# Optimization experiments

Hardware: AMD Instinct MI355X
Metric: run time of the kernel (lower is better)

The kernel has to match this reference:

```python
import jax, jax.numpy as jnp
import numpy as np

# Inverse Haar synthesis filters [LL, LH, HL, HH], each 2x2, shape [4,2,2]
_INV_FILTERS = jnp.array([
    [[0.5, 0.5], [0.5, 0.5]],    # LL
    [[-0.5, -0.5], [0.5, 0.5]],  # LH
    [[-0.5, 0.5], [-0.5, 0.5]],  # HL
    [[0.5, -0.5], [-0.5, 0.5]],  # HH
], dtype=jnp.float32)


def _iwt(ll, hf, filt):
    # ll: [B,C,H,W]; hf: [B,3C,H,W] -> recon [B,C,2H,2W]
    B, C, H, W = ll.shape
    # interleave: per channel c -> [ll_c, hf_{3c..3c+2}*2-1], shape [B,C,4,H,W]
    res = jnp.concatenate([ll[:, :, None], hf.reshape(B, C, 3, H, W) * 2.0 - 1.0], axis=2)
    # stride-2 2x2 transpose conv == scatter each pixel into a 2x2 block
    out = jnp.einsum('bckhw,kpq->bchpwq', res, filt)  # [B,C,H,2,W,2]
    return out.reshape(B, C, 2 * H, 2 * W)


def setup_inputs() -> dict:
    key = jax.random.key(0)
    k1, k2, k3, k4 = jax.random.split(key, 4)
    B, in_ch = 16, 64
    fused = jax.random.normal(k1, (B, in_ch, 128, 128), dtype=jnp.float32)
    hf1 = jax.random.uniform(k2, (B, 9, 256, 256), dtype=jnp.float32)
    hf2 = jax.random.uniform(k3, (B, 9, 128, 128), dtype=jnp.float32)
    conv_w = jax.random.normal(k4, (3, in_ch, 3, 3), dtype=jnp.float32) * 0.05
    conv_b = jnp.zeros((3,), dtype=jnp.float32)
    return {"fused": fused, "hf1": hf1, "hf2": hf2, "conv_w": conv_w, "conv_b": conv_b}


def reference(fused, hf1, hf2, conv_w, conv_b):
    # recov: Conv2d(in_ch, 3, 3, padding=1) + Tanh
    y = jax.lax.conv_general_dilated(
        fused, conv_w, window_strides=(1, 1), padding=((1, 1), (1, 1)),
        dimension_numbers=('NCHW', 'OIHW', 'NCHW'))
    ll_ref = jnp.tanh(y + conv_b[None, :, None, None])  # [B,3,128,128]
    # multi_iwt over reversed coeffs: curr starts at coarsest ll (= ll_ref)
    curr = _iwt(ll_ref, hf2, _INV_FILTERS)  # [B,3,256,256]
    curr = _iwt(curr, hf1, _INV_FILTERS)    # [B,3,512,512]
    return curr
```

## Files before the change

kernel.cpp:

```cpp
#include <hip/hip_runtime.h>
#include <cmath>


#define H1 128
#define W1 128
#define H2 256
#define W2 256
#define H3 512
#define W3 512
#define IN_CH 64

__global__ __launch_bounds__(256) void conv_tanh_kernel(
    const float* __restrict__ fused,
    const float* __restrict__ cw,
    const float* __restrict__ cb,
    float* __restrict__ ll)
{
    const int tx = threadIdx.x;
    const int ty = threadIdx.y;
    const int h  = blockIdx.y * 4 + ty;
    const int b  = blockIdx.z;
    const int w0 = tx * 2;

    float acc[3][2];
    #pragma unroll
    for (int oc = 0; oc < 3; ++oc) { acc[oc][0] = 0.f; acc[oc][1] = 0.f; }

    const float* fb = fused + ((size_t)b * IN_CH) * H1 * W1;

    for (int ic = 0; ic < IN_CH; ++ic) {
        const float* fc = fb + ic * H1 * W1;
        float v[3][4];
        #pragma unroll
        for (int r = 0; r < 3; ++r) {
            const int hh = h + r - 1;
            const bool hv = (hh >= 0) && (hh < H1);
            const float* row = fc + hh * W1;
            v[r][0] = (hv && (w0 > 0)) ? row[w0 - 1] : 0.f;
            if (hv) {
                float2 m = *(const float2*)(row + w0);
                v[r][1] = m.x; v[r][2] = m.y;
            } else {
                v[r][1] = 0.f; v[r][2] = 0.f;
            }
            v[r][3] = (hv && ((w0 + 2) < W1)) ? row[w0 + 2] : 0.f;
        }
        #pragma unroll
        for (int oc = 0; oc < 3; ++oc) {
            const float* wp = cw + (oc * IN_CH + ic) * 9;
            #pragma unroll
            for (int kh = 0; kh < 3; ++kh) {
                #pragma unroll
                for (int kw = 0; kw < 3; ++kw) {
                    const float wv = wp[kh * 3 + kw];
                    acc[oc][0] = fmaf(v[kh][kw],     wv, acc[oc][0]);
                    acc[oc][1] = fmaf(v[kh][kw + 1], wv, acc[oc][1]);
                }
            }
        }
    }

    #pragma unroll
    for (int oc = 0; oc < 3; ++oc) {
        const float bv = cb[oc];
        float2 o;
        o.x = tanhf(acc[oc][0] + bv);
        o.y = tanhf(acc[oc][1] + bv);
        *(float2*)(ll + (((size_t)b * 3 + oc) * H1 + h) * W1 + w0) = o;
    }
}

__global__ __launch_bounds__(256) void iwt2_kernel(
    const float* __restrict__ ll,
    const float* __restrict__ hf2,
    const float* __restrict__ hf1,
    float* __restrict__ out)
{
    const int idx = blockIdx.x * 256 + threadIdx.x;
    const int w = idx & (W1 - 1);
    const int h = (idx >> 7) & (H1 - 1);
    const int rest = idx >> 14;
    const int c = rest % 3;
    const int b = rest / 3;

    const float llv = ll[(((size_t)b * 3 + c) * H1 + h) * W1 + w];

    const float* h2p = hf2 + (((size_t)b * 9 + 3 * c) * H1 + h) * W1 + w;
    const float a2 = h2p[0]           * 2.f - 1.f;
    const float b2 = h2p[H1 * W1]     * 2.f - 1.f;
    const float c2 = h2p[2 * H1 * W1] * 2.f - 1.f;

    float mid[2][2];
    mid[0][0] = 0.5f * (llv - a2 - b2 + c2);
    mid[0][1] = 0.5f * (llv - a2 + b2 - c2);
    mid[1][0] = 0.5f * (llv + a2 - b2 - c2);
    mid[1][1] = 0.5f * (llv + a2 + b2 + c2);

    const float* h1b = hf1 + ((size_t)b * 9 + 3 * c) * H2 * W2;
    float* ob = out + (((size_t)b * 3 + c) * H3) * W3;

    #pragma unroll
    for (int p = 0; p < 2; ++p) {
        const int Hr = 2 * h + p;
        const float* rowp = h1b + Hr * W2 + 2 * w;
        const float2 a1 = *(const float2*)(rowp);
        const float2 b1 = *(const float2*)(rowp + H2 * W2);
        const float2 c1 = *(const float2*)(rowp + 2 * H2 * W2);
        const float ax = a1.x * 2.f - 1.f, ay = a1.y * 2.f - 1.f;
        const float bx = b1.x * 2.f - 1.f, by = b1.y * 2.f - 1.f;
        const float cx = c1.x * 2.f - 1.f, cy = c1.y * 2.f - 1.f;
        #pragma unroll
        for (int r = 0; r < 2; ++r) {
            const float sr = r ? 1.f : -1.f;
            float4 o;
            o.x = 0.5f * (mid[p][0] + sr * ax - bx - sr * cx);
            o.y = 0.5f * (mid[p][0] + sr * ax + bx + sr * cx);
            o.z = 0.5f * (mid[p][1] + sr * ay - by - sr * cy);
            o.w = 0.5f * (mid[p][1] + sr * ay + by + sr * cy);
            *(float4*)(ob + (4 * h + 2 * p + r) * W3 + 4 * w) = o;
        }
    }
}

extern "C" void kernel_launch(void* const* d_in, const int* in_sizes, int n_in,
                              void* d_out, int out_size, void* d_ws, size_t ws_size,
                              hipStream_t stream) {
    (void)in_sizes; (void)n_in; (void)out_size; (void)ws_size;
    const float* fused = (const float*)d_in[0];
    const float* hf1   = (const float*)d_in[1];
    const float* hf2   = (const float*)d_in[2];
    const float* cw    = (const float*)d_in[3];
    const float* cb    = (const float*)d_in[4];
    float* out = (float*)d_out;
    float* ll  = (float*)d_ws;

    dim3 cblk(64, 4, 1);
    dim3 cgrd(1, H1 / 4, 16);
    conv_tanh_kernel<<<cgrd, cblk, 0, stream>>>(fused, cw, cb, ll);

    const int total = 16 * 3 * H1 * W1;
    iwt2_kernel<<<total / 256, 256, 0, stream>>>(ll, hf2, hf1, out);
}
```

Baseline: 197.4 us.

## Split conv input channels across blocks and fuse reduction+tanh into IWT kernel

The conv kernel is split over four input-channel chunks, so the grid grows from 512 to 2048 blocks and occupancy improves. Each chunk writes raw partial sums to workspace, and the IWT kernel adds them, applies bias and tanh, then runs the two inverse Haar stages. The IWT kernel now handles two low-res pixels per thread with wider vector loads and stores, and the conv loop double-buffers its row loads. The cost is extra workspace traffic for four partial planes, plus a fallback path when the workspace is too small.

Measured after the change: 330.0 us. 67.1% more time.

```diff
diff --git a/kernel.cpp b/kernel.cpp
--- a/kernel.cpp
+++ b/kernel.cpp
@@ -9,45 +9,50 @@
 #define H3 512
 #define W3 512
 #define IN_CH 64
+#define NB 16
+#define PLANE (H1 * W1)
+#define LLSZ (NB * 3 * PLANE)
 
-__global__ __launch_bounds__(256) void conv_tanh_kernel(
+template <int ICP>
+__global__ __launch_bounds__(256, 8) void conv_part_kernel(
     const float* __restrict__ fused,
     const float* __restrict__ cw,
-    const float* __restrict__ cb,
-    float* __restrict__ ll)
+    float* __restrict__ part)
 {
-    const int tx = threadIdx.x;
-    const int ty = threadIdx.y;
-    const int h  = blockIdx.y * 4 + ty;
-    const int b  = blockIdx.z;
-    const int w0 = tx * 2;
+    const int tx    = threadIdx.x;
+    const int ty    = threadIdx.y;
+    const int chunk = blockIdx.x;
+    const int h     = blockIdx.y * 4 + ty;
+    const int b     = blockIdx.z;
+    const int w0    = tx * 2;
 
     float acc[3][2];
     #pragma unroll
     for (int oc = 0; oc < 3; ++oc) { acc[oc][0] = 0.f; acc[oc][1] = 0.f; }
 
-    const float* fb = fused + ((size_t)b * IN_CH) * H1 * W1;
+    const float* fc = fused + ((size_t)b * IN_CH + chunk * ICP) * PLANE;
 
-    for (int ic = 0; ic < IN_CH; ++ic) {
-        const float* fc = fb + ic * H1 * W1;
-        float v[3][4];
+    float va[3][4], vb[3][4];
+
+    auto ldrow = [&](float v[3][4], const float* p) {
         #pragma unroll
         for (int r = 0; r < 3; ++r) {
             const int hh = h + r - 1;
-            const bool hv = (hh >= 0) && (hh < H1);
-            const float* row = fc + hh * W1;
+            const bool hv = ((unsigned)hh) < (unsigned)H1;
+            const float* row = p + hh * W1;
             v[r][0] = (hv && (w0 > 0)) ? row[w0 - 1] : 0.f;
             if (hv) {
                 float2 m = *(const float2*)(row + w0);
                 v[r][1] = m.x; v[r][2] = m.y;
-            } else {
-                v[r][1] = 0.f; v[r][2] = 0.f;
-            }
+            } else { v[r][1] = 0.f; v[r][2] = 0.f; }
             v[r][3] = (hv && ((w0 + 2) < W1)) ? row[w0 + 2] : 0.f;
         }
+    };
+
+    auto comp = [&](const float v[3][4], int ic) {
         #pragma unroll
         for (int oc = 0; oc < 3; ++oc) {
-            const float* wp = cw + (oc * IN_CH + ic) * 9;
+            const float* wp = cw + (oc * IN_CH + chunk * ICP + ic) * 9;
             #pragma unroll
             for (int kh = 0; kh < 3; ++kh) {
                 #pragma unroll
@@ -58,66 +63,98 @@
                 }
             }
         }
+    };
+
+    ldrow(va, fc);
+    #pragma unroll 2
+    for (int ic = 0; ic < ICP; ic += 2) {
+        ldrow(vb, fc + (size_t)(ic + 1) * PLANE);
+        comp(va, ic);
+        if (ic + 2 < ICP) ldrow(va, fc + (size_t)(ic + 2) * PLANE);
+        comp(vb, ic + 1);
     }
 
+    const size_t base = (size_t)chunk * LLSZ + (((size_t)b * 3) * H1 + h) * W1 + w0;
     #pragma unroll
     for (int oc = 0; oc < 3; ++oc) {
-        const float bv = cb[oc];
-        float2 o;
-        o.x = tanhf(acc[oc][0] + bv);
-        o.y = tanhf(acc[oc][1] + bv);
-        *(float2*)(ll + (((size_t)b * 3 + oc) * H1 + h) * W1 + w0) = o;
+        float2 o; o.x = acc[oc][0]; o.y = acc[oc][1];
+        *(float2*)(part + base + (size_t)oc * PLANE) = o;
     }
 }
 
+template <int NCHUNK>
 __global__ __launch_bounds__(256) void iwt2_kernel(
-    const float* __restrict__ ll,
+    const float* __restrict__ part,
+    const float* __restrict__ cb,
     const float* __restrict__ hf2,
     const float* __restrict__ hf1,
     float* __restrict__ out)
 {
     const int idx = blockIdx.x * 256 + threadIdx.x;
-    const int w = idx & (W1 - 1);
-    const int h = (idx >> 7) & (H1 - 1);
-    const int rest = idx >> 14;
+    const int w0 = (idx & 63) * 2;
+    const int h  = (idx >> 6) & (H1 - 1);
+    const int rest = idx >> 13;
     const int c = rest % 3;
     const int b = rest / 3;
 
-    const float llv = ll[(((size_t)b * 3 + c) * H1 + h) * W1 + w];
+    const size_t llbase = (((size_t)(b * 3 + c)) * H1 + h) * W1 + w0;
+    float sx = 0.f, sy = 0.f;
+    #pragma unroll
+    for (int k = 0; k < NCHUNK; ++k) {
+        float2 p = *(const float2*)(part + (size_t)k * LLSZ + llbase);
+        sx += p.x; sy += p.y;
+    }
+    const float bias = cb[c];
+    float llv[2];
+    llv[0] = tanhf(sx + bias);
+    llv[1] = tanhf(sy + bias);
 
-    const float* h2p = hf2 + (((size_t)b * 9 + 3 * c) * H1 + h) * W1 + w;
-    const float a2 = h2p[0]           * 2.f - 1.f;
-    const float b2 = h2p[H1 * W1]     * 2.f - 1.f;
-    const float c2 = h2p[2 * H1 * W1] * 2.f - 1.f;
+    const float* h2p = hf2 + (((size_t)b * 9 + 3 * c) * H1 + h) * W1 + w0;
+    float mid[2][2][2];
+    #pragma unroll
+    for (int j = 0; j < 1; ++j) {}
+    {
+        const float2 A = *(const float2*)(h2p);
+        const float2 Bv = *(const float2*)(h2p + PLANE);
+        const float2 Cv = *(const float2*)(h2p + 2 * PLANE);
+        const float a[2] = { A.x * 2.f - 1.f,  A.y * 2.f - 1.f };
+        const float bq[2] = { Bv.x * 2.f - 1.f, Bv.y * 2.f - 1.f };
+        const float cq[2] = { Cv.x * 2.f - 1.f, Cv.y * 2.f - 1.f };
+        #pragma unroll
+        for (int x = 0; x < 2; ++x) {
+            mid[x][0][0] = 0.5f * (llv[x] - a[x] - bq[x] + cq[x]);
+            mid[x][0][1] = 0.5f * (llv[x] - a[x] + bq[x] - cq[x]);
+            mid[x][1][0] = 0.5f * (llv[x] + a[x] - bq[x] - cq[x]);
+            mid[x][1][1] = 0.5f * (llv[x] + a[x] + bq[x] + cq[x]);
+        }
+    }
 
-    float mid[2][2];
-    mid[0][0] = 0.5f * (llv - a2 - b2 + c2);
-    mid[0][1] = 0.5f * (llv - a2 + b2 - c2);
-    mid[1][0] = 0.5f * (llv + a2 - b2 - c2);
-    mid[1][1] = 0.5f * (llv + a2 + b2 + c2);
-
-    const float* h1b = hf1 + ((size_t)b * 9 + 3 * c) * H2 * W2;
-    float* ob = out + (((size_t)b * 3 + c) * H3) * W3;
+    const float* h1b = hf1 + ((size_t)b * 9 + 3 * c) * (H2 * W2);
+    float* ob = out + ((size_t)(b * 3 + c)) * (H3 * W3);
 
     #pragma unroll
     for (int p = 0; p < 2; ++p) {
         const int Hr = 2 * h + p;
-        const float* rowp = h1b + Hr * W2 + 2 * w;
-        const float2 a1 = *(const float2*)(rowp);
-        const float2 b1 = *(const float2*)(rowp + H2 * W2);
-        const float2 c1 = *(const float2*)(rowp + 2 * H2 * W2);
-        const float ax = a1.x * 2.f - 1.f, ay = a1.y * 2.f - 1.f;
-        const float bx = b1.x * 2.f - 1.f, by = b1.y * 2.f - 1.f;
-        const float cx = c1.x * 2.f - 1.f, cy = c1.y * 2.f - 1.f;
+        const float* rowp = h1b + (size_t)Hr * W2 + 2 * w0;
+        float4 A = *(const float4*)(rowp);
+        float4 Bv = *(const float4*)(rowp + H2 * W2);
+        float4 Cv = *(const float4*)(rowp + 2 * H2 * W2);
+        const float a[2][2]  = { {A.x * 2.f - 1.f,  A.y * 2.f - 1.f},  {A.z * 2.f - 1.f,  A.w * 2.f - 1.f} };
+        const float bb[2][2] = { {Bv.x * 2.f - 1.f, Bv.y * 2.f - 1.f}, {Bv.z * 2.f - 1.f, Bv.w * 2.f - 1.f} };
+        const float cc[2][2] = { {Cv.x * 2.f - 1.f, Cv.y * 2.f - 1.f}, {Cv.z * 2.f - 1.f, Cv.w * 2.f - 1.f} };
         #pragma unroll
         for (int r = 0; r < 2; ++r) {
             const float sr = r ? 1.f : -1.f;
-            float4 o;
-            o.x = 0.5f * (mid[p][0] + sr * ax - bx - sr * cx);
-            o.y = 0.5f * (mid[p][0] + sr * ax + bx + sr * cx);
-            o.z = 0.5f * (mid[p][1] + sr * ay - by - sr * cy);
-            o.w = 0.5f * (mid[p][1] + sr * ay + by + sr * cy);
-            *(float4*)(ob + (4 * h + 2 * p + r) * W3 + 4 * w) = o;
+            float* orow = ob + (size_t)(4 * h + 2 * p + r) * W3 + 4 * w0;
+            #pragma unroll
+            for (int x = 0; x < 2; ++x) {
+                float4 o;
+                o.x = 0.5f * (mid[x][p][0] + sr * a[x][0] - bb[x][0] - sr * cc[x][0]);
+                o.y = 0.5f * (mid[x][p][0] + sr * a[x][0] + bb[x][0] + sr * cc[x][0]);
+                o.z = 0.5f * (mid[x][p][1] + sr * a[x][1] - bb[x][1] - sr * cc[x][1]);
+                o.w = 0.5f * (mid[x][p][1] + sr * a[x][1] + bb[x][1] + sr * cc[x][1]);
+                *(float4*)(orow + 4 * x) = o;
+            }
         }
     }
 }
@@ -125,19 +162,26 @@
 extern "C" void kernel_launch(void* const* d_in, const int* in_sizes, int n_in,
                               void* d_out, int out_size, void* d_ws, size_t ws_size,
                               hipStream_t stream) {
-    (void)in_sizes; (void)n_in; (void)out_size; (void)ws_size;
+    (void)in_sizes; (void)n_in; (void)out_size;
     const float* fused = (const float*)d_in[0];
     const float* hf1   = (const float*)d_in[1];
     const float* hf2   = (const float*)d_in[2];
     const float* cw    = (const float*)d_in[3];
     const float* cb    = (const float*)d_in[4];
-    float* out = (float*)d_out;
-    float* ll  = (float*)d_ws;
+    float* out  = (float*)d_out;
+    float* part = (float*)d_ws;
 
+    const size_t need4 = (size_t)4 * LLSZ * sizeof(float);
     dim3 cblk(64, 4, 1);
-    dim3 cgrd(1, H1 / 4, 16);
-    conv_tanh_kernel<<<cgrd, cblk, 0, stream>>>(fused, cw, cb, ll);
+    const int iwtBlocks = (NB * 3 * H1 * (W1 / 2)) / 256;
 
-    const int total = 16 * 3 * H1 * W1;
-    iwt2_kernel<<<total / 256, 256, 0, stream>>>(ll, hf2, hf1, out);
+    if (ws_size >= need4) {
+        dim3 cgrd(4, H1 / 4, NB);
+        conv_part_kernel<16><<<cgrd, cblk, 0, stream>>>(fused, cw, part);
+        iwt2_kernel<4><<<iwtBlocks, 256, 0, stream>>>(part, cb, hf2, hf1, out);
+    } else {
+        dim3 cgrd(1, H1 / 4, NB);
+        conv_part_kernel<64><<<cgrd, cblk, 0, stream>>>(fused, cw, part);
+        iwt2_kernel<1><<<iwtBlocks, 256, 0, stream>>>(part, cb, hf2, hf1, out);
+    }
 }
```
